# Performance work log

Measured on AMD Instinct MI355X. Metric: run time of the kernel, lower is better.

Reference implementation:

```python
import jax, jax.numpy as jnp
import numpy as np

B, L = 2, 1024
D_MODEL = 1024
D_STATE = 16
K = 3            # conv kernel (odd so padding=(K-1)//2 preserves L)
EXPAND = 1       # module is only shape-consistent with d_inner == d_model
D_INNER = D_MODEL * EXPAND


def setup_inputs() -> dict:
    key = jax.random.key(0)
    ks = jax.random.split(key, 10)
    s = 0.02
    x = jax.random.normal(ks[0], (B, L, D_MODEL), dtype=jnp.float32)
    W_in = jax.random.normal(ks[1], (D_MODEL, 2 * D_INNER), dtype=jnp.float32) * s
    conv_w = jax.random.normal(ks[2], (D_INNER, 1, K), dtype=jnp.float32) * s  # depthwise OIH
    W_B = jax.random.normal(ks[3], (D_INNER, D_STATE), dtype=jnp.float32) * s
    W_C = jax.random.normal(ks[4], (D_INNER, D_STATE), dtype=jnp.float32) * s
    W_delta = jax.random.normal(ks[5], (D_INNER, D_MODEL), dtype=jnp.float32) * s
    delta_base = jax.random.normal(ks[6], (D_MODEL,), dtype=jnp.float32)
    W_tau = jax.random.normal(ks[7], (D_MODEL, D_MODEL), dtype=jnp.float32) * s
    A_log = jnp.tile(jnp.log(jnp.arange(1, D_STATE + 1, dtype=jnp.float32)), (D_MODEL, 1))
    W_out = jax.random.normal(ks[8], (D_INNER, D_MODEL), dtype=jnp.float32) * s
    return {"x": x, "W_in": W_in, "conv_w": conv_w, "W_B": W_B, "W_C": W_C,
            "W_delta": W_delta, "delta_base": delta_base, "W_tau": W_tau,
            "A_log": A_log, "W_out": W_out}


def _silu(v):
    return v * jax.nn.sigmoid(v)


def _mamba_fwd(x, W_in, conv_w, W_B, W_C, W_delta, delta_base, W_tau, A_log, W_out):
    residual = x
    z = x @ W_in                               # [B,L,2*D_INNER]
    val, gate = jnp.split(z, 2, axis=-1)
    # depthwise causal-ish conv1d (padding=(K-1)//2)
    v = jnp.transpose(val, (0, 2, 1))          # [B,C,L]
    v = jax.lax.conv_general_dilated(
        v, conv_w, window_strides=(1,), padding=[((K - 1) // 2, (K - 1) // 2)],
        dimension_numbers=("NCH", "OIH", "NCH"), feature_group_count=D_INNER)
    val = jnp.transpose(_silu(v), (0, 2, 1))   # [B,L,D_INNER]

    B_proj = val @ W_B                          # [B,L,N]
    C_proj = val @ W_C                          # [B,L,N]
    combined_delta = val @ W_delta + delta_base # [B,L,D_MODEL]
    Delta = jax.nn.softplus(combined_delta @ W_tau)  # [B,L,D]

    A = -jnp.exp(A_log)                         # [D,N]
    dA = Delta[..., None] * A                   # [B,L,D,N]
    A_bar = jnp.exp(dA)
    B_bar = jnp.expm1(dA) / (dA + 1e-6) * Delta[..., None] * B_proj[:, :, None, :]

    def step(h, inp):
        a_t, b_t, c_t, u_t = inp                # a/b:[B,D,N], c:[B,N], u:[B,D]
        h = a_t * h + b_t * u_t[..., None]
        y_t = jnp.sum(h * c_t[:, None, :], axis=-1)  # [B,D]
        return h, y_t

    h0 = jnp.zeros((x.shape[0], D_INNER, D_STATE), dtype=x.dtype)
    xs = (jnp.moveaxis(A_bar, 1, 0), jnp.moveaxis(B_bar, 1, 0),
          jnp.moveaxis(C_proj, 1, 0), jnp.moveaxis(val, 1, 0))
    _, ys = jax.lax.scan(step, h0, xs)          # ys: [L,B,D]
    y = jnp.moveaxis(ys, 0, 1)                  # [B,L,D]

    out = (y * _silu(gate)) @ W_out + residual  # [B,L,D_MODEL]
    return out


def reference(x, W_in, conv_w, W_B, W_C, W_delta, delta_base, W_tau, A_log, W_out):
    return _mamba_fwd(x, W_in, conv_w, W_B, W_C, W_delta, delta_base, W_tau, A_log, W_out)
```

## Files before the change

### kernel.cpp

```cpp
#include <hip/hip_runtime.h>
#include <math.h>

#define BB 2
#define LL 1024
#define DM 1024
#define DI 1024
#define DS 16
#define ROWS (BB * LL)
#define CH 16
#define NCH (LL / CH)
#define NP 1152
#define NF 1152

typedef unsigned short ushort_t;
typedef __attribute__((ext_vector_type(8))) short short8;
typedef __attribute__((ext_vector_type(4))) float f32x4;
typedef __attribute__((ext_vector_type(4))) float f4;
typedef __attribute__((ext_vector_type(4))) ushort_t us4;

static __device__ __forceinline__ float sp_f(float x) {
    return fmaxf(x, 0.f) + log1pf(expf(-fabsf(x)));
}
static __device__ __forceinline__ ushort_t f2bf(float f) {
    unsigned u = __float_as_uint(f);
    u += 0x7fffu + ((u >> 16) & 1u);
    return (ushort_t)(u >> 16);
}
static __device__ __forceinline__ float bf2f(ushort_t s) {
    return __uint_as_float(((unsigned)s) << 16);
}

#define SWZ(L) ((L) ^ ((((L) >> 7) & 1) << 4) ^ ((((L) >> 8) & 1) << 5))

static __device__ __forceinline__ void gl_lds16(const void* g, void* l) {
    __builtin_amdgcn_global_load_lds(
        (const __attribute__((address_space(1))) unsigned int*)g,
        (__attribute__((address_space(3))) unsigned int*)l, 16, 0, 0);
}

template <int ACT, bool HAS_BIAS, bool HAS_RES, bool OUTBF, int PROJMODE>
__global__ __launch_bounds__(256) void gemm_bf_k(
    const ushort_t* __restrict__ A, const ushort_t* __restrict__ Bt,
    const float* __restrict__ bias, const float* __restrict__ res,
    void* __restrict__ Cout, float* __restrict__ BpO, float* __restrict__ CpO,
    int M, int N, int K, int ldc)
{
    __shared__ __align__(16) char lsa[2][4096];
    __shared__ __align__(16) char lsb[2][8192];

    const int tid = threadIdx.x;
    const int lane = tid & 63;
    const int w = tid >> 6;
    const int wr = w >> 1, wc = w & 1;

    int wg = blockIdx.y * gridDim.x + blockIdx.x;
    const int nwg = gridDim.x * gridDim.y;
    wg = (wg & 7) * (nwg >> 3) + (wg >> 3);
    const int bx = wg % gridDim.x, by = wg / gridDim.x;
    const int row0 = by * 64, col0 = bx * 128;

    const int rl = lane & 15, q = lane >> 4;

    const char* gA;
    {
        int L = SWZ(w * 1024 + lane * 16);
        gA = (const char*)A + ((size_t)(row0 + (L >> 6)) * K) * 2 + (L & 63);
    }
    const char* gB[2];
#pragma unroll
    for (int j = 0; j < 2; ++j) {
        int L = SWZ((w * 2 + j) * 1024 + lane * 16);
        gB[j] = (const char*)Bt + ((size_t)(col0 + (L >> 6)) * K) * 2 + (L & 63);
    }

    int LA[2], LB[4];
#pragma unroll
    for (int m = 0; m < 2; ++m) LA[m] = SWZ((wr * 32 + m * 16 + rl) * 64 + q * 16);
#pragma unroll
    for (int n = 0; n < 4; ++n) LB[n] = SWZ((wc * 64 + n * 16 + rl) * 64 + q * 16);

    f32x4 acc[2][4] = {};
    const int NT = K >> 5;

    gl_lds16(gA, &lsa[0][w * 1024]);
    gl_lds16(gB[0], &lsb[0][(w * 2) * 1024]);
    gl_lds16(gB[1], &lsb[0][(w * 2 + 1) * 1024]);
    __syncthreads();

    int cur = 0;
    for (int kt = 0; kt < NT; ++kt) {
        if (kt + 1 < NT) {
            const int kb = (kt + 1) * 64;
            gl_lds16(gA + kb, &lsa[cur ^ 1][w * 1024]);
            gl_lds16(gB[0] + kb, &lsb[cur ^ 1][(w * 2) * 1024]);
            gl_lds16(gB[1] + kb, &lsb[cur ^ 1][(w * 2 + 1) * 1024]);
        }
        short8 af[2], bfr[4];
#pragma unroll
        for (int m = 0; m < 2; ++m) af[m] = *(const short8*)(&lsa[cur][LA[m]]);
#pragma unroll
        for (int n = 0; n < 4; ++n) bfr[n] = *(const short8*)(&lsb[cur][LB[n]]);
#pragma unroll
        for (int m = 0; m < 2; ++m)
#pragma unroll
            for (int n = 0; n < 4; ++n)
                acc[m][n] = __builtin_amdgcn_mfma_f32_16x16x32_bf16(
                    af[m], bfr[n], acc[m][n], 0, 0, 0);
        __syncthreads();
        cur ^= 1;
    }

    float bia[4];
#pragma unroll
    for (int n = 0; n < 4; ++n) {
        int c = col0 + wc * 64 + n * 16 + rl;
        bia[n] = (HAS_BIAS && c < DM) ? bias[c] : 0.f;
    }
#pragma unroll
    for (int m = 0; m < 2; ++m) {
#pragma unroll
        for (int n = 0; n < 4; ++n) {
            int c = col0 + wc * 64 + n * 16 + rl;
#pragma unroll
            for (int i = 0; i < 4; ++i) {
                int r = row0 + wr * 32 + m * 16 + q * 4 + i;
                float v = acc[m][n][i];
                if (PROJMODE == 1 && c >= DM) {
                    if (c < DM + DS)          BpO[(size_t)r * DS + (c - DM)] = v;
                    else if (c < DM + 2 * DS) CpO[(size_t)r * DS + (c - DM - DS)] = v;
                } else if (PROJMODE == 2 && c >= DM) {
                    if (c == DM) BpO[r] = v;
                } else {
                    v += bia[n];
                    if (ACT == 1) v = sp_f(v);
                    if (HAS_RES) v += res[(size_t)r * ldc + c];
                    if (OUTBF) ((ushort_t*)Cout)[(size_t)r * ldc + c] = f2bf(v);
                    else       ((float*)Cout)[(size_t)r * ldc + c] = v;
                }
            }
        }
    }
}

static __device__ __forceinline__ void tconv_body(
    const float* __restrict__ in, ushort_t* __restrict__ out,
    int K, int N, int n0, int k0, float (*t)[33], int tid)
{
    int lx = tid & 31, ly = tid >> 5;
#pragma unroll
    for (int i = 0; i < 32; i += 8)
        t[ly + i][lx] = in[(size_t)(k0 + ly + i) * N + n0 + lx];
    __syncthreads();
#pragma unroll
    for (int i = 0; i < 32; i += 8)
        out[(size_t)(n0 + ly + i) * K + k0 + lx] = f2bf(t[lx][ly + i]);
}

__global__ __launch_bounds__(256) void prep_k(
    const float* __restrict__ x, const float* __restrict__ W_in,
    const float* __restrict__ W_B, const float* __restrict__ W_C,
    const float* __restrict__ W_delta, const float* __restrict__ db,
    const float* __restrict__ W_tau, const float* __restrict__ W_out,
    ushort_t* __restrict__ x_bf, ushort_t* __restrict__ WinT,
    ushort_t* __restrict__ WtT, ushort_t* __restrict__ WoT,
    ushort_t* __restrict__ WdX, ushort_t* __restrict__ WdcT)
{
    __shared__ float t[32][33];
    const int blk = blockIdx.x;
    const int tid = threadIdx.x;
    if (blk < 2048) {
        int i = blk * 256 + tid;
        f4 v = ((const f4*)x)[i];
        us4 o; o.x = f2bf(v.x); o.y = f2bf(v.y); o.z = f2bf(v.z); o.w = f2bf(v.w);
        ((us4*)x_bf)[i] = o;
    } else if (blk < 3072) {
        int i = (blk - 2048) * 256 + tid;
        f4 v = ((const f4*)W_delta)[i];
        us4 o; o.x = f2bf(v.x); o.y = f2bf(v.y); o.z = f2bf(v.z); o.w = f2bf(v.w);
        ((us4*)WdX)[i] = o;
    } else if (blk < 3584) {
        int i = (blk - 3072) * 256 + tid;
        int k = i & 1023, r = i >> 10;
        WdX[(size_t)(1024 + r) * 1024 + k] = (r == 0) ? f2bf(db[k]) : (ushort_t)0;
    } else if (blk < 5632) {
        int tau = blk - 3584;
        tconv_body(W_in, WinT, 1024, 2048, (tau & 63) * 32, (tau >> 6) * 32, t, tid);
    } else if (blk < 6656) {
        int tau = blk - 5632;
        tconv_body(W_tau, WtT, 1024, 1024, (tau & 31) * 32, (tau >> 5) * 32, t, tid);
    } else if (blk < 7680) {
        int tau = blk - 6656;
        tconv_body(W_out, WoT, 1024, 1024, (tau & 31) * 32, (tau >> 5) * 32, t, tid);
    } else {
        int i = (blk - 7680) * 256 + tid;
        int k = i & 1023, r = i >> 10;
        ushort_t v = 0;
        if (r < DS)          v = f2bf(W_B[(size_t)k * DS + r]);
        else if (r < 2 * DS) v = f2bf(W_C[(size_t)k * DS + (r - DS)]);
        WdcT[(size_t)(1024 + r) * 1024 + k] = v;
    }
}

__global__ __launch_bounds__(256) void conv_silu_k(
    const ushort_t* __restrict__ z_bf, const float* __restrict__ cw,
    ushort_t* __restrict__ val_bf)
{
    int t = blockIdx.x * 256 + threadIdx.x;
    int c0 = (t & 255) * 4;
    int row = t >> 8;
    int l = row & (LL - 1);
    const ushort_t* zr = z_bf + (size_t)row * (2 * DI) + c0;
    us4 zz = {0, 0, 0, 0};
    us4 vm = (l > 0)      ? *(const us4*)(zr - 2 * DI) : zz;
    us4 v0 = *(const us4*)(zr);
    us4 vp = (l < LL - 1) ? *(const us4*)(zr + 2 * DI) : zz;
    const f4* wp = (const f4*)(cw + (size_t)c0 * 3);
    f4 w0 = wp[0], w1 = wp[1], w2 = wp[2];
    float w[12];
#pragma unroll
    for (int k = 0; k < 4; ++k) { w[k] = w0[k]; w[4 + k] = w1[k]; w[8 + k] = w2[k]; }
    us4 o;
#pragma unroll
    for (int j = 0; j < 4; ++j) {
        float s = bf2f(vm[j]) * w[3 * j] + bf2f(v0[j]) * w[3 * j + 1]
                + bf2f(vp[j]) * w[3 * j + 2];
        float si = s / (1.f + __expf(-s));
        o[j] = f2bf(si);
    }
    *(us4*)(val_bf + (size_t)row * DI + c0) = o;
}

__global__ __launch_bounds__(256) void scan_p1_k(
    const ushort_t* __restrict__ Del_bf, const ushort_t* __restrict__ val_bf,
    const float* __restrict__ Bp, const float* __restrict__ A_log,
    float* __restrict__ aprod, float* __restrict__ hloc)
{
    int t = blockIdx.x * 256 + threadIdx.x;
    int d = t & (DI - 1);
    int c = (t >> 10) & (NCH - 1);
    int b = t >> 16;

    float Adn[DS], ci[DS];
    const f4* alp = (const f4*)(A_log + (size_t)d * DS);
#pragma unroll
    for (int j = 0; j < 4; ++j) {
        f4 al = alp[j];
#pragma unroll
        for (int k = 0; k < 4; ++k) {
            float a = -__expf(al[k]);
            Adn[j * 4 + k] = a;
            ci[j * 4 + k] = 1.0f / a;
        }
    }
    int row0 = b * LL + c * CH;
    const ushort_t* Dp = Del_bf + (size_t)row0 * DI + d;
    const ushort_t* up = val_bf + (size_t)row0 * DI + d;
    const f4* bp = (const f4*)(Bp + (size_t)row0 * DS);

    float h[DS];
#pragma unroll
    for (int n = 0; n < DS; ++n) h[n] = 0.f;
    float sdv = 0.f;

#pragma unroll 2
    for (int l = 0; l < CH; ++l) {
        float dv = bf2f(Dp[(size_t)l * DI]);
        float u  = bf2f(up[(size_t)l * DI]);
        f4 q0 = bp[l * 4 + 0], q1 = bp[l * 4 + 1], q2 = bp[l * 4 + 2], q3 = bp[l * 4 + 3];
        float bn[DS];
#pragma unroll
        for (int k = 0; k < 4; ++k) {
            bn[k] = q0[k]; bn[4 + k] = q1[k]; bn[8 + k] = q2[k]; bn[12 + k] = q3[k];
        }
        sdv += dv;
#pragma unroll
        for (int n = 0; n < DS; ++n) {
            float a  = __expf(dv * Adn[n]);
            float tt = (ci[n] * bn[n]) * u;
            float s  = h[n] + tt;
            h[n] = fmaf(a, s, -tt);
        }
    }
    size_t o = (((size_t)b * NCH + c) * DI + d) * DS;
#pragma unroll
    for (int j = 0; j < 4; ++j) {
        f4 hv, av;
#pragma unroll
        for (int k = 0; k < 4; ++k) {
            hv[k] = h[j * 4 + k];
            av[k] = __expf(sdv * Adn[j * 4 + k]);
        }
        *(f4*)(hloc + o + j * 4) = hv;
        *(f4*)(aprod + o + j * 4) = av;
    }
}

__global__ __launch_bounds__(256) void scan_p2_k(
    const float* __restrict__ aprod, const float* __restrict__ hloc,
    float* __restrict__ hin)
{
    int t = blockIdx.x * 256 + threadIdx.x;
    int dn = t & (DI * DS - 1);
    int b = t >> 14;
    float h = 0.f;
    size_t base = (size_t)b * NCH * DI * DS + dn;
#pragma unroll 4
    for (int c = 0; c < NCH; ++c) {
        size_t idx = base + (size_t)c * (DI * DS);
        hin[idx] = h;
        h = fmaf(aprod[idx], h, hloc[idx]);
    }
}

__global__ __launch_bounds__(256) void scan_p3_k(
    const ushort_t* __restrict__ Del_bf, const ushort_t* __restrict__ val_bf,
    const float* __restrict__ Bp, const float* __restrict__ Cp,
    const float* __restrict__ A_log, const float* __restrict__ hin,
    const ushort_t* __restrict__ z_bf, ushort_t* __restrict__ g_bf)
{
    int t = blockIdx.x * 256 + threadIdx.x;
    int d = t & (DI - 1);
    int c = (t >> 10) & (NCH - 1);
    int b = t >> 16;

    float Adn[DS], ci[DS];
    const f4* alp = (const f4*)(A_log + (size_t)d * DS);
#pragma unroll
    for (int j = 0; j < 4; ++j) {
        f4 al = alp[j];
#pragma unroll
        for (int k = 0; k < 4; ++k) {
            float a = -__expf(al[k]);
            Adn[j * 4 + k] = a;
            ci[j * 4 + k] = 1.0f / a;
        }
    }
    int row0 = b * LL + c * CH;
    const ushort_t* Dp = Del_bf + (size_t)row0 * DI + d;
    const ushort_t* up = val_bf + (size_t)row0 * DI + d;
    const ushort_t* zp = z_bf + (size_t)row0 * (2 * DI) + DI + d;
    const f4* bp = (const f4*)(Bp + (size_t)row0 * DS);
    const f4* cp = (const f4*)(Cp + (size_t)row0 * DS);
    ushort_t* gp = g_bf + (size_t)row0 * DI + d;

    float h[DS];
    size_t o = (((size_t)b * NCH + c) * DI + d) * DS;
#pragma unroll
    for (int j = 0; j < 4; ++j) {
        f4 hv = *(const f4*)(hin + o + j * 4);
#pragma unroll
        for (int k = 0; k < 4; ++k) h[j * 4 + k] = hv[k];
    }

#pragma unroll 2
    for (int l = 0; l < CH; ++l) {
        float dv = bf2f(Dp[(size_t)l * DI]);
        float u  = bf2f(up[(size_t)l * DI]);
        f4 q0 = bp[l * 4 + 0], q1 = bp[l * 4 + 1], q2 = bp[l * 4 + 2], q3 = bp[l * 4 + 3];
        f4 r0 = cp[l * 4 + 0], r1 = cp[l * 4 + 1], r2 = cp[l * 4 + 2], r3 = cp[l * 4 + 3];
        float bn[DS], cn[DS];
#pragma unroll
        for (int k = 0; k < 4; ++k) {
            bn[k] = q0[k]; bn[4 + k] = q1[k]; bn[8 + k] = q2[k]; bn[12 + k] = q3[k];
            cn[k] = r0[k]; cn[4 + k] = r1[k]; cn[8 + k] = r2[k]; cn[12 + k] = r3[k];
        }
        float psum = 0.f;
#pragma unroll
        for (int n = 0; n < DS; ++n) {
            float a  = __expf(dv * Adn[n]);
            float tt = (ci[n] * bn[n]) * u;
            float s  = h[n] + tt;
            h[n] = fmaf(a, s, -tt);
            psum = fmaf(h[n], cn[n], psum);
        }
        float zg = bf2f(zp[(size_t)l * 2 * DI]);
        float si = zg / (1.f + __expf(-zg));
        gp[(size_t)l * DI] = f2bf(psum * si);
    }
}

extern "C" void kernel_launch(void* const* d_in, const int* in_sizes, int n_in,
                              void* d_out, int out_size, void* d_ws, size_t ws_size,
                              hipStream_t stream)
{
    (void)in_sizes; (void)n_in; (void)out_size; (void)ws_size;

    const float* x        = (const float*)d_in[0];
    const float* W_in     = (const float*)d_in[1];
    const float* conv_w   = (const float*)d_in[2];
    const float* W_B      = (const float*)d_in[3];
    const float* W_C      = (const float*)d_in[4];
    const float* W_delta  = (const float*)d_in[5];
    const float* delta_b  = (const float*)d_in[6];
    const float* W_tau    = (const float*)d_in[7];
    const float* A_log    = (const float*)d_in[8];
    const float* W_out    = (const float*)d_in[9];
    float* out = (float*)d_out;

    const size_t M1 = 1024 * 1024;
    ushort_t* us = (ushort_t*)d_ws;
    ushort_t* z_bf   = us;
    ushort_t* val_bf = us + 4 * M1;
    ushort_t* Del_bf = us + 6 * M1;
    ushort_t* x_bf   = us + 8 * M1;
    ushort_t* g_bf   = us + 10 * M1;
    ushort_t* WinT   = us + 12 * M1;
    ushort_t* WoT    = us + 14 * M1;
    ushort_t* WtT    = us + 15 * M1;
    ushort_t* WdX    = us + 16 * M1;
    ushort_t* WdcT   = WdX + (size_t)NF * 1024;
    float* fb    = (float*)(us + 20 * M1);
    float* Bp    = fb;
    float* Cp    = fb + (size_t)ROWS * DS;
    float* b2    = fb + 2 * (size_t)ROWS * DS;
    float* aprod = b2 + 1024;
    float* hloc  = aprod + 2 * M1;
    float* hin   = hloc + 2 * M1;

    prep_k<<<8192, 256, 0, stream>>>(x, W_in, W_B, W_C, W_delta, delta_b,
                                     W_tau, W_out, x_bf, WinT, WtT, WoT, WdX, WdcT);

    gemm_bf_k<0, false, false, true, 2><<<dim3(NF / 128, DM / 64), 256, 0, stream>>>(
        WtT, WdX, nullptr, nullptr, WdcT, b2, nullptr, DM, NF, DM, DM);

    gemm_bf_k<0, false, false, true, 0><<<dim3(2 * DI / 128, ROWS / 64), 256, 0, stream>>>(
        x_bf, WinT, nullptr, nullptr, z_bf, nullptr, nullptr, ROWS, 2 * DI, DM, 2 * DI);

    conv_silu_k<<<(ROWS * DI / 4) / 256, 256, 0, stream>>>(z_bf, conv_w, val_bf);

    gemm_bf_k<1, true, false, true, 1><<<dim3(NP / 128, ROWS / 64), 256, 0, stream>>>(
        val_bf, WdcT, b2, nullptr, Del_bf, Bp, Cp, ROWS, NP, DI, DM);

    scan_p1_k<<<(BB * NCH * DI) / 256, 256, 0, stream>>>(
        Del_bf, val_bf, Bp, A_log, aprod, hloc);
    scan_p2_k<<<(BB * DI * DS) / 256, 256, 0, stream>>>(aprod, hloc, hin);
    scan_p3_k<<<(BB * NCH * DI) / 256, 256, 0, stream>>>(
        Del_bf, val_bf, Bp, Cp, A_log, hin, z_bf, g_bf);

    gemm_bf_k<0, false, true, false, 0><<<dim3(DM / 128, ROWS / 64), 256, 0, stream>>>(
        g_bf, WoT, nullptr, x, out, nullptr, nullptr, ROWS, DM, DI, DM);
}
```

Before: 239.9 us.

## Double GEMM K-tile to 64 and overlap prefetch with explicit vmcnt waits

Doubles the bf16 GEMM K-tile from 32 to 64 elements, with a wider XOR swizzle for the 128-byte LDS rows, so each iteration issues twice as many MFMAs per barrier. The two __syncthreads per iteration are replaced by inline s_waitcnt vmcnt(6) plus s_barrier, so the next tile's global-to-LDS loads stay in flight while the current tile is consumed. This is meant to cut barrier and loop overhead and hide load latency. In exchange, LDS use doubles, which may reduce occupancy, and correctness now depends on the hand-written vmcnt counting.

```diff
diff --git a/kernel.cpp b/kernel.cpp
--- a/kernel.cpp
+++ b/kernel.cpp
@@ -30,7 +30,7 @@
     return __uint_as_float(((unsigned)s) << 16);
 }
 
-#define SWZ(L) ((L) ^ ((((L) >> 7) & 1) << 4) ^ ((((L) >> 8) & 1) << 5))
+#define SWZ(L) ((L) ^ ((((L) >> 7) & 7) << 4))
 
 static __device__ __forceinline__ void gl_lds16(const void* g, void* l) {
     __builtin_amdgcn_global_load_lds(
@@ -45,8 +45,8 @@
     void* __restrict__ Cout, float* __restrict__ BpO, float* __restrict__ CpO,
     int M, int N, int K, int ldc)
 {
-    __shared__ __align__(16) char lsa[2][4096];
-    __shared__ __align__(16) char lsb[2][8192];
+    __shared__ __align__(16) char lsa[2][8192];
+    __shared__ __align__(16) char lsb[2][16384];
 
     const int tid = threadIdx.x;
     const int lane = tid & 63;
@@ -61,52 +61,73 @@
 
     const int rl = lane & 15, q = lane >> 4;
 
-    const char* gA;
-    {
-        int L = SWZ(w * 1024 + lane * 16);
-        gA = (const char*)A + ((size_t)(row0 + (L >> 6)) * K) * 2 + (L & 63);
-    }
-    const char* gB[2];
+    const char* gA[2];
 #pragma unroll
     for (int j = 0; j < 2; ++j) {
         int L = SWZ((w * 2 + j) * 1024 + lane * 16);
-        gB[j] = (const char*)Bt + ((size_t)(col0 + (L >> 6)) * K) * 2 + (L & 63);
-    }
-
-    int LA[2], LB[4];
-#pragma unroll
-    for (int m = 0; m < 2; ++m) LA[m] = SWZ((wr * 32 + m * 16 + rl) * 64 + q * 16);
-#pragma unroll
-    for (int n = 0; n < 4; ++n) LB[n] = SWZ((wc * 64 + n * 16 + rl) * 64 + q * 16);
+        gA[j] = (const char*)A + ((size_t)(row0 + (L >> 7)) * K) * 2 + (L & 127);
+    }
+    const char* gB[4];
+#pragma unroll
+    for (int j = 0; j < 4; ++j) {
+        int L = SWZ((w * 4 + j) * 1024 + lane * 16);
+        gB[j] = (const char*)Bt + ((size_t)(col0 + (L >> 7)) * K) * 2 + (L & 127);
+    }
+
+    int LA[2][2], LB[4][2];
+#pragma unroll
+    for (int m = 0; m < 2; ++m)
+#pragma unroll
+        for (int kk = 0; kk < 2; ++kk)
+            LA[m][kk] = SWZ((wr * 32 + m * 16 + rl) * 128 + kk * 64 + q * 16);
+#pragma unroll
+    for (int n = 0; n < 4; ++n)
+#pragma unroll
+        for (int kk = 0; kk < 2; ++kk)
+            LB[n][kk] = SWZ((wc * 64 + n * 16 + rl) * 128 + kk * 64 + q * 16);
 
     f32x4 acc[2][4] = {};
-    const int NT = K >> 5;
-
-    gl_lds16(gA, &lsa[0][w * 1024]);
-    gl_lds16(gB[0], &lsb[0][(w * 2) * 1024]);
-    gl_lds16(gB[1], &lsb[0][(w * 2 + 1) * 1024]);
-    __syncthreads();
+    const int NT = K >> 6;
+
+#pragma unroll
+    for (int j = 0; j < 2; ++j) gl_lds16(gA[j], &lsa[0][(w * 2 + j) * 1024]);
+#pragma unroll
+    for (int j = 0; j < 4; ++j) gl_lds16(gB[j], &lsb[0][(w * 4 + j) * 1024]);
 
     int cur = 0;
     for (int kt = 0; kt < NT; ++kt) {
         if (kt + 1 < NT) {
-            const int kb = (kt + 1) * 64;
-            gl_lds16(gA + kb, &lsa[cur ^ 1][w * 1024]);
-            gl_lds16(gB[0] + kb, &lsb[cur ^ 1][(w * 2) * 1024]);
-            gl_lds16(gB[1] + kb, &lsb[cur ^ 1][(w * 2 + 1) * 1024]);
-        }
-        short8 af[2], bfr[4];
-#pragma unroll
-        for (int m = 0; m < 2; ++m) af[m] = *(const short8*)(&lsa[cur][LA[m]]);
-#pragma unroll
-        for (int n = 0; n < 4; ++n) bfr[n] = *(const short8*)(&lsb[cur][LB[n]]);
+            const int kb = (kt + 1) * 128;
+#pragma unroll
+            for (int j = 0; j < 2; ++j)
+                gl_lds16(gA[j] + kb, &lsa[cur ^ 1][(w * 2 + j) * 1024]);
+#pragma unroll
+            for (int j = 0; j < 4; ++j)
+                gl_lds16(gB[j] + kb, &lsb[cur ^ 1][(w * 4 + j) * 1024]);
+            asm volatile("s_waitcnt vmcnt(6)\n\ts_barrier" ::: "memory");
+        } else {
+            asm volatile("s_waitcnt vmcnt(0)\n\ts_barrier" ::: "memory");
+        }
+        short8 af[2][2], bfr[4][2];
 #pragma unroll
         for (int m = 0; m < 2; ++m)
 #pragma unroll
-            for (int n = 0; n < 4; ++n)
-                acc[m][n] = __builtin_amdgcn_mfma_f32_16x16x32_bf16(
-                    af[m], bfr[n], acc[m][n], 0, 0, 0);
-        __syncthreads();
+            for (int kk = 0; kk < 2; ++kk)
+                af[m][kk] = *(const short8*)(&lsa[cur][LA[m][kk]]);
+#pragma unroll
+        for (int n = 0; n < 4; ++n)
+#pragma unroll
+            for (int kk = 0; kk < 2; ++kk)
+                bfr[n][kk] = *(const short8*)(&lsb[cur][LB[n][kk]]);
+#pragma unroll
+        for (int kk = 0; kk < 2; ++kk)
+#pragma unroll
+            for (int m = 0; m < 2; ++m)
+#pragma unroll
+                for (int n = 0; n < 4; ++n)
+                    acc[m][n] = __builtin_amdgcn_mfma_f32_16x16x32_bf16(
+                        af[m][kk], bfr[n][kk], acc[m][n], 0, 0, 0);
+        asm volatile("s_barrier" ::: "memory");
         cur ^= 1;
     }
 
```

Result: faster. 231.2 us (-3.6%).
